# Performance work log

Measured on AMD Instinct MI355X. Metric: run time of the kernel, lower is better.

The kernel has to match this reference:

```python
import jax, jax.numpy as jnp
import numpy as np

B, L, F = 512, 30, 64
N_LEADERS, MAX_LAG = 500, 10
H, TOP_K = 64, 5
SCALE = float(H) ** 0.5


def setup_inputs() -> dict:
    key = jax.random.key(0)
    ks = jax.random.split(key, 16)
    s = 0.05
    return {
        "target_seq": jax.random.normal(ks[0], (B, L, F), jnp.float32),
        "leader_raw_features": jax.random.normal(ks[1], (B, N_LEADERS, MAX_LAG, F), jnp.float32),
        # LSTM params (torch gate order i,f,g,o)
        "W_ih": jax.random.normal(ks[2], (4 * H, F), jnp.float32) * s,
        "W_hh": jax.random.normal(ks[3], (4 * H, H), jnp.float32) * s,
        "b_ih": jax.random.normal(ks[4], (4 * H,), jnp.float32) * s,
        "b_hh": jax.random.normal(ks[5], (4 * H,), jnp.float32) * s,
        # attention projections (bias-free)
        "W_Q": jax.random.normal(ks[6], (H, H), jnp.float32) * s,
        "W_K": jax.random.normal(ks[7], (H, F), jnp.float32) * s,
        # predictor MLP: F->H, H->H//2, H//2->1
        "Wp1": jax.random.normal(ks[8], (H, F), jnp.float32) * s,
        "bp1": jax.random.normal(ks[9], (H,), jnp.float32) * s,
        "Wp2": jax.random.normal(ks[10], (H // 2, H), jnp.float32) * s,
        "bp2": jax.random.normal(ks[11], (H // 2,), jnp.float32) * s,
        "Wp3": jax.random.normal(ks[12], (1, H // 2), jnp.float32) * s,
        "bp3": jax.random.normal(ks[13], (1,), jnp.float32) * s,
    }


def _lstm_last_hidden(x, W_ih, W_hh, b_ih, b_hh):
    # x: [B, L, F] -> last hidden state [B, H]
    b = x.shape[0]
    h0 = jnp.zeros((b, W_hh.shape[1]), x.dtype)

    def step(carry, xt):
        h, c = carry
        gates = xt @ W_ih.T + h @ W_hh.T + b_ih + b_hh  # [B, 4H]
        i, f, g, o = jnp.split(gates, 4, axis=-1)
        i = jax.nn.sigmoid(i)
        f = jax.nn.sigmoid(f)
        g = jnp.tanh(g)
        o = jax.nn.sigmoid(o)
        c = f * c + i * g
        h = o * jnp.tanh(c)
        return (h, c), None

    (h_last, _), _ = jax.lax.scan(step, (h0, h0), jnp.swapaxes(x, 0, 1))
    return h_last


def reference(target_seq, leader_raw_features, W_ih, W_hh, b_ih, b_hh,
              W_Q, W_K, Wp1, bp1, Wp2, bp2, Wp3, bp3):
    b = target_seq.shape[0]
    n_leaders, max_lag, feat = leader_raw_features.shape[1:]

    h_last = _lstm_last_hidden(target_seq, W_ih, W_hh, b_ih, b_hh)  # [B,H]
    query = h_last @ W_Q.T  # [B,H]

    # attn[b,n,l] = sum_h query[b,h] * (W_K @ raw[b,n,l])_h, fused to avoid
    # materializing the [B,N,LAG,H] key tensor.
    attn = jnp.einsum('bnlf,hf,bh->bnl', leader_raw_features, W_K, query) / SCALE

    flat_attn = attn.reshape(b, n_leaders * max_lag)
    k = min(TOP_K, flat_attn.shape[1])
    top_values, top_idx = jax.lax.top_k(flat_attn, k)  # [B,k]
    leader_idx = top_idx // max_lag
    lag_idx = top_idx % max_lag
    top_k_indices = jnp.stack([leader_idx, lag_idx], axis=-1)  # [B,k,2]
    top_k_scores = jax.nn.softmax(top_values, axis=-1)  # [B,k]

    raw_flat = leader_raw_features.reshape(b, n_leaders * max_lag, feat)
    selected = jnp.take_along_axis(raw_flat, top_idx[:, :, None], axis=1)  # [B,k,F]
    weighted = jnp.einsum('bkf,bk->bf', selected, top_k_scores)  # [B,F]

    # predictor MLP (dropout is identity in eval)
    h1 = jax.nn.relu(weighted @ Wp1.T + bp1)
    h2 = jax.nn.relu(h1 @ Wp2.T + bp2)
    pred = h2 @ Wp3.T + bp3  # [B,1]
    return pred, top_k_indices, top_k_scores, attn
```

## Files before the change

### kernel.cpp

```cpp
#include <hip/hip_runtime.h>
#include <math.h>

#define B_SZ   512
#define L_SEQ  30
#define F_DIM  64
#define N_LEAD 500
#define MAXLAG 10
#define H_DIM  64
#define NROWS  5000
#define TOPK   5

#define OFF_IDX   512
#define OFF_SCORE 5632
#define OFF_ATTN  8192

__device__ __forceinline__ float fast_sigmoid(float x) {
    return 1.f / (1.f + __expf(-x));
}
__device__ __forceinline__ float fast_tanh(float x) {
    float ax = fabsf(x);
    float t  = __expf(-2.f * ax);
    float r  = (1.f - t) / (1.f + t);
    return copysignf(r, x);
}
__device__ __forceinline__ float sfl(float v) {
    return __uint_as_float(__builtin_amdgcn_readfirstlane(__float_as_uint(v)));
}

__device__ __forceinline__ float dot16(const float4* __restrict__ w,
                                       const float4* __restrict__ v) {
    float a0 = 0.f, a1 = 0.f, a2 = 0.f, a3 = 0.f;
#pragma unroll
    for (int k = 0; k < 16; k += 4) {
        a0 += w[k+0].x*v[k+0].x + w[k+0].y*v[k+0].y + w[k+0].z*v[k+0].z + w[k+0].w*v[k+0].w;
        a1 += w[k+1].x*v[k+1].x + w[k+1].y*v[k+1].y + w[k+1].z*v[k+1].z + w[k+1].w*v[k+1].w;
        a2 += w[k+2].x*v[k+2].x + w[k+2].y*v[k+2].y + w[k+2].z*v[k+2].z + w[k+2].w*v[k+2].w;
        a3 += w[k+3].x*v[k+3].x + w[k+3].y*v[k+3].y + w[k+3].z*v[k+3].z + w[k+3].w*v[k+3].w;
    }
    return (a0 + a1) + (a2 + a3);
}

__global__ __launch_bounds__(256) void lstm_kq_kernel(
    const float* __restrict__ x,
    const float* __restrict__ W_ih,
    const float* __restrict__ W_hh,
    const float* __restrict__ b_ih,
    const float* __restrict__ b_hh,
    const float* __restrict__ W_Q,
    const float* __restrict__ W_K,
    float* __restrict__ kq)
{
    __shared__ __align__(16) float xs[L_SEQ * F_DIM];
    __shared__ __align__(16) float hs[H_DIM];
    __shared__ __align__(16) float gates[256];

    const int b = blockIdx.x;
    const int t = threadIdx.x;

    for (int i = t; i < L_SEQ * F_DIM; i += 256)
        xs[i] = x[b * L_SEQ * F_DIM + i];
    if (t < H_DIM) hs[t] = 0.f;

    float4 wih[16], whh[16];
    const float4* wihp = (const float4*)(W_ih + t * 64);
    const float4* whhp = (const float4*)(W_hh + t * 64);
#pragma unroll
    for (int k = 0; k < 16; ++k) { wih[k] = wihp[k]; whh[k] = whhp[k]; }
    const float bsum = b_ih[t] + b_hh[t];

    float c = 0.f;
    __syncthreads();

    float gx = bsum + dot16(wih, (const float4*)xs);

    for (int step = 0; step < L_SEQ; ++step) {
        float g = gx + dot16(whh, (const float4*)hs);
        gates[t] = g;
        __syncthreads();
        if (t < H_DIM) {
            float ig = fast_sigmoid(gates[t]);
            float fg = fast_sigmoid(gates[t + 64]);
            float gg = fast_tanh(gates[t + 128]);
            float og = fast_sigmoid(gates[t + 192]);
            c = fg * c + ig * gg;
            hs[t] = og * fast_tanh(c);
        }
        if (step + 1 < L_SEQ)
            gx = bsum + dot16(wih, (const float4*)(xs + (step + 1) * F_DIM));
        __syncthreads();
    }

    if (t < H_DIM)
        gates[t] = dot16((const float4*)(W_Q + t * 64), (const float4*)hs);
    __syncthreads();
    if (t < F_DIM) {
        float a0 = 0.f, a1 = 0.f;
        for (int h = 0; h < H_DIM; h += 2) {
            a0 += gates[h]     * W_K[h * F_DIM + t];
            a1 += gates[h + 1] * W_K[(h + 1) * F_DIM + t];
        }
        kq[b * F_DIM + t] = a0 + a1;
    }
}

__global__ __launch_bounds__(512, 8) void fused_attn_topk_kernel(
    const float* __restrict__ raw,
    const float* __restrict__ kq,
    const float* __restrict__ Wp1, const float* __restrict__ bp1,
    const float* __restrict__ Wp2, const float* __restrict__ bp2,
    const float* __restrict__ Wp3, const float* __restrict__ bp3,
    float* __restrict__ out)
{
    __shared__ float av[NROWS];
    __shared__ float redv[8];
    __shared__ int   redi[8];
    __shared__ float topv[TOPK];
    __shared__ int   topi[TOPK];
    __shared__ float sc[TOPK];
    __shared__ __align__(16) float wsum[64];
    __shared__ __align__(16) float h1[64];
    __shared__ float h2[32];

    const int b = blockIdx.x, t = threadIdx.x;

    const float* kqp = kq + b * 64;
#define LQ(i) const float q##i##x = sfl(kqp[4*(i)+0]), q##i##y = sfl(kqp[4*(i)+1]), \
                          q##i##z = sfl(kqp[4*(i)+2]), q##i##w = sfl(kqp[4*(i)+3]);
    LQ(0) LQ(1) LQ(2) LQ(3) LQ(4) LQ(5) LQ(6) LQ(7)
    LQ(8) LQ(9) LQ(10) LQ(11) LQ(12) LQ(13) LQ(14) LQ(15)
#undef LQ

    float* attn_g = out + OFF_ATTN + (size_t)b * NROWS;
    const float4* p = (const float4*)raw + ((size_t)b * NROWS + t) * 16;

#define DOT4(acc, v, i) acc += v.x*q##i##x + v.y*q##i##y + v.z*q##i##z + v.w*q##i##w;
#define BODY(r) { \
    float4 v0=p[0],v1=p[1],v2=p[2],v3=p[3],v4=p[4],v5=p[5],v6=p[6],v7=p[7]; \
    float s0=0.f,s1=0.f,s2=0.f,s3=0.f; \
    DOT4(s0,v0,0) DOT4(s1,v1,1) DOT4(s2,v2,2) DOT4(s3,v3,3) \
    DOT4(s0,v4,4) DOT4(s1,v5,5) DOT4(s2,v6,6) DOT4(s3,v7,7) \
    v0=p[8];v1=p[9];v2=p[10];v3=p[11];v4=p[12];v5=p[13];v6=p[14];v7=p[15]; \
    DOT4(s0,v0,8)  DOT4(s1,v1,9)  DOT4(s2,v2,10) DOT4(s3,v3,11) \
    DOT4(s0,v4,12) DOT4(s1,v5,13) DOT4(s2,v6,14) DOT4(s3,v7,15) \
    float s = ((s0+s1)+(s2+s3)) * 0.125f; \
    av[r] = s; attn_g[r] = s; }

    int r = t;
#pragma unroll 1
    for (int pass = 0; pass < 9; ++pass) {
        BODY(r)
        r += 512; p += 512 * 16;
    }
    if (r < NROWS) { BODY(r) }
#undef BODY
#undef DOT4
    __syncthreads();

    for (int pp = 0; pp < TOPK; ++pp) {
        float bv = -INFINITY; int bi = 0x7fffffff;
        for (int i = t; i < NROWS; i += 512) {
            float v = av[i];
            if (v > bv || (v == bv && i < bi)) { bv = v; bi = i; }
        }
#pragma unroll
        for (int m = 32; m >= 1; m >>= 1) {
            float ov = __shfl_xor(bv, m);
            int   oi = __shfl_xor(bi, m);
            if (ov > bv || (ov == bv && oi < bi)) { bv = ov; bi = oi; }
        }
        if ((t & 63) == 0) { redv[t >> 6] = bv; redi[t >> 6] = bi; }
        __syncthreads();
        if (t == 0) {
            for (int w = 1; w < 8; ++w)
                if (redv[w] > bv || (redv[w] == bv && redi[w] < bi)) { bv = redv[w]; bi = redi[w]; }
            topv[pp] = bv; topi[pp] = bi;
            av[bi] = -INFINITY;
        }
        __syncthreads();
    }

    if (t == 0) {
        float mx = topv[0];
        float e[TOPK], s = 0.f;
#pragma unroll
        for (int k = 0; k < TOPK; ++k) { e[k] = __expf(topv[k] - mx); s += e[k]; }
        float inv = 1.f / s;
#pragma unroll
        for (int k = 0; k < TOPK; ++k) {
            sc[k] = e[k] * inv;
            out[OFF_IDX + b * 10 + 2 * k]     = (float)(topi[k] / MAXLAG);
            out[OFF_IDX + b * 10 + 2 * k + 1] = (float)(topi[k] % MAXLAG);
            out[OFF_SCORE + b * TOPK + k]     = sc[k];
        }
    }
    __syncthreads();

    if (t < 64) {
        float acc = 0.f;
#pragma unroll
        for (int k = 0; k < TOPK; ++k)
            acc += sc[k] * raw[((size_t)b * NROWS + topi[k]) * 64 + t];
        wsum[t] = acc;
    }
    __syncthreads();
    if (t < 64) {
        float a = bp1[t];
        const float4* w = (const float4*)(Wp1 + t * 64);
        const float4* v = (const float4*)wsum;
#pragma unroll
        for (int k = 0; k < 16; ++k)
            a += w[k].x*v[k].x + w[k].y*v[k].y + w[k].z*v[k].z + w[k].w*v[k].w;
        h1[t] = fmaxf(a, 0.f);
    }
    __syncthreads();
    if (t < 32) {
        float a = bp2[t];
        const float4* w = (const float4*)(Wp2 + t * 64);
        const float4* v = (const float4*)h1;
#pragma unroll
        for (int k = 0; k < 16; ++k)
            a += w[k].x*v[k].x + w[k].y*v[k].y + w[k].z*v[k].z + w[k].w*v[k].w;
        h2[t] = fmaxf(a, 0.f);
    }
    __syncthreads();
    if (t == 0) {
        float a = bp3[0];
#pragma unroll
        for (int f = 0; f < 32; ++f) a += Wp3[f] * h2[f];
        out[b] = a;
    }
}

extern "C" void kernel_launch(void* const* d_in, const int* in_sizes, int n_in,
                              void* d_out, int out_size, void* d_ws, size_t ws_size,
                              hipStream_t stream) {
    const float* target = (const float*)d_in[0];
    const float* raw    = (const float*)d_in[1];
    const float* W_ih   = (const float*)d_in[2];
    const float* W_hh   = (const float*)d_in[3];
    const float* b_ih   = (const float*)d_in[4];
    const float* b_hh   = (const float*)d_in[5];
    const float* W_Q    = (const float*)d_in[6];
    const float* W_K    = (const float*)d_in[7];
    const float* Wp1    = (const float*)d_in[8];
    const float* bp1    = (const float*)d_in[9];
    const float* Wp2    = (const float*)d_in[10];
    const float* bp2    = (const float*)d_in[11];
    const float* Wp3    = (const float*)d_in[12];
    const float* bp3    = (const float*)d_in[13];

    float* out = (float*)d_out;
    float* kq  = (float*)d_ws;

    hipLaunchKernelGGL(lstm_kq_kernel, dim3(B_SZ), dim3(256), 0, stream,
                       target, W_ih, W_hh, b_ih, b_hh, W_Q, W_K, kq);
    hipLaunchKernelGGL(fused_attn_topk_kernel, dim3(B_SZ), dim3(512), 0, stream,
                       raw, kq, Wp1, bp1, Wp2, bp2, Wp3, bp3, out);
}
```

Baseline: 207.2 us.

## Split fused attention/top-k kernel into streaming attn kernel and top-k MLP kernel

The fused per-batch kernel is split in two. The first computes attention scores over the leader features with 4 blocks per batch row, giving 2048 blocks of 256 threads, and writes them to the output buffer. The second reloads those scores into shared memory and runs top-k, softmax and the MLP. The goal is more parallelism and occupancy for the bandwidth-bound streaming pass, which no longer carries a 20KB shared-memory footprint. The cost is an extra kernel launch and a write and re-read of the 10MB attention array.

```diff
diff --git a/kernel.cpp b/kernel.cpp
--- a/kernel.cpp
+++ b/kernel.cpp
@@ -103,17 +103,63 @@
     }
 }
 
-__global__ __launch_bounds__(512, 8) void fused_attn_topk_kernel(
+#define RPB 1250
+__global__ __launch_bounds__(256, 8) void attn_stream_kernel(
+    const float4* __restrict__ raw,
+    const float* __restrict__ kq,
+    float* __restrict__ attn)
+{
+    const int b = blockIdx.x >> 2;
+    const int q = blockIdx.x & 3;
+    const int t = threadIdx.x;
+
+    const float* kqp = kq + b * 64;
+#define LQ(i) const float q##i##x = sfl(kqp[4*(i)+0]), q##i##y = sfl(kqp[4*(i)+1]), \
+                          q##i##z = sfl(kqp[4*(i)+2]), q##i##w = sfl(kqp[4*(i)+3]);
+    LQ(0) LQ(1) LQ(2) LQ(3) LQ(4) LQ(5) LQ(6) LQ(7)
+    LQ(8) LQ(9) LQ(10) LQ(11) LQ(12) LQ(13) LQ(14) LQ(15)
+#undef LQ
+
+    const int row0 = q * RPB;
+    const float4* p = raw + ((size_t)b * NROWS + row0 + t) * 16;
+    float*       ag = attn + (size_t)b * NROWS + row0 + t;
+
+#define DOT4(acc, v, i) acc += v.x*q##i##x + v.y*q##i##y + v.z*q##i##z + v.w*q##i##w;
+#define BODY() { \
+    float4 v0=p[0],v1=p[1],v2=p[2],v3=p[3]; \
+    float s0=0.f,s1=0.f,s2=0.f,s3=0.f; \
+    DOT4(s0,v0,0) DOT4(s1,v1,1) DOT4(s2,v2,2) DOT4(s3,v3,3) \
+    v0=p[4];v1=p[5];v2=p[6];v3=p[7]; \
+    DOT4(s0,v0,4) DOT4(s1,v1,5) DOT4(s2,v2,6) DOT4(s3,v3,7) \
+    v0=p[8];v1=p[9];v2=p[10];v3=p[11]; \
+    DOT4(s0,v0,8) DOT4(s1,v1,9) DOT4(s2,v2,10) DOT4(s3,v3,11) \
+    v0=p[12];v1=p[13];v2=p[14];v3=p[15]; \
+    DOT4(s0,v0,12) DOT4(s1,v1,13) DOT4(s2,v2,14) DOT4(s3,v3,15) \
+    *ag = ((s0+s1)+(s2+s3)) * 0.125f; }
+
+#pragma unroll 1
+    for (int i = 0; i < 4; ++i) {
+        BODY()
+        p += 256 * 16; ag += 256;
+    }
+    if (t < RPB - 1024) {
+        BODY()
+    }
+#undef BODY
+#undef DOT4
+}
+
+__global__ __launch_bounds__(256) void topk_mlp_kernel(
+    const float* __restrict__ attn,
     const float* __restrict__ raw,
-    const float* __restrict__ kq,
     const float* __restrict__ Wp1, const float* __restrict__ bp1,
     const float* __restrict__ Wp2, const float* __restrict__ bp2,
     const float* __restrict__ Wp3, const float* __restrict__ bp3,
     float* __restrict__ out)
 {
-    __shared__ float av[NROWS];
-    __shared__ float redv[8];
-    __shared__ int   redi[8];
+    __shared__ __align__(16) float av[NROWS];
+    __shared__ float redv[4];
+    __shared__ int   redi[4];
     __shared__ float topv[TOPK];
     __shared__ int   topi[TOPK];
     __shared__ float sc[TOPK];
@@ -123,42 +169,14 @@
 
     const int b = blockIdx.x, t = threadIdx.x;
 
-    const float* kqp = kq + b * 64;
-#define LQ(i) const float q##i##x = sfl(kqp[4*(i)+0]), q##i##y = sfl(kqp[4*(i)+1]), \
-                          q##i##z = sfl(kqp[4*(i)+2]), q##i##w = sfl(kqp[4*(i)+3]);
-    LQ(0) LQ(1) LQ(2) LQ(3) LQ(4) LQ(5) LQ(6) LQ(7)
-    LQ(8) LQ(9) LQ(10) LQ(11) LQ(12) LQ(13) LQ(14) LQ(15)
-#undef LQ
-
-    float* attn_g = out + OFF_ATTN + (size_t)b * NROWS;
-    const float4* p = (const float4*)raw + ((size_t)b * NROWS + t) * 16;
-
-#define DOT4(acc, v, i) acc += v.x*q##i##x + v.y*q##i##y + v.z*q##i##z + v.w*q##i##w;
-#define BODY(r) { \
-    float4 v0=p[0],v1=p[1],v2=p[2],v3=p[3],v4=p[4],v5=p[5],v6=p[6],v7=p[7]; \
-    float s0=0.f,s1=0.f,s2=0.f,s3=0.f; \
-    DOT4(s0,v0,0) DOT4(s1,v1,1) DOT4(s2,v2,2) DOT4(s3,v3,3) \
-    DOT4(s0,v4,4) DOT4(s1,v5,5) DOT4(s2,v6,6) DOT4(s3,v7,7) \
-    v0=p[8];v1=p[9];v2=p[10];v3=p[11];v4=p[12];v5=p[13];v6=p[14];v7=p[15]; \
-    DOT4(s0,v0,8)  DOT4(s1,v1,9)  DOT4(s2,v2,10) DOT4(s3,v3,11) \
-    DOT4(s0,v4,12) DOT4(s1,v5,13) DOT4(s2,v6,14) DOT4(s3,v7,15) \
-    float s = ((s0+s1)+(s2+s3)) * 0.125f; \
-    av[r] = s; attn_g[r] = s; }
-
-    int r = t;
-#pragma unroll 1
-    for (int pass = 0; pass < 9; ++pass) {
-        BODY(r)
-        r += 512; p += 512 * 16;
-    }
-    if (r < NROWS) { BODY(r) }
-#undef BODY
-#undef DOT4
+    const float4* ain = (const float4*)(attn + (size_t)b * NROWS);
+    float4* av4 = (float4*)av;
+    for (int i = t; i < NROWS / 4; i += 256) av4[i] = ain[i];
     __syncthreads();
 
     for (int pp = 0; pp < TOPK; ++pp) {
         float bv = -INFINITY; int bi = 0x7fffffff;
-        for (int i = t; i < NROWS; i += 512) {
+        for (int i = t; i < NROWS; i += 256) {
             float v = av[i];
             if (v > bv || (v == bv && i < bi)) { bv = v; bi = i; }
         }
@@ -171,7 +189,7 @@
         if ((t & 63) == 0) { redv[t >> 6] = bv; redi[t >> 6] = bi; }
         __syncthreads();
         if (t == 0) {
-            for (int w = 1; w < 8; ++w)
+            for (int w = 1; w < 4; ++w)
                 if (redv[w] > bv || (redv[w] == bv && redi[w] < bi)) { bv = redv[w]; bi = redi[w]; }
             topv[pp] = bv; topi[pp] = bi;
             av[bi] = -INFINITY;
@@ -249,11 +267,14 @@
     const float* Wp3    = (const float*)d_in[12];
     const float* bp3    = (const float*)d_in[13];
 
-    float* out = (float*)d_out;
-    float* kq  = (float*)d_ws;
+    float* out      = (float*)d_out;
+    float* kq       = (float*)d_ws;
+    float* attn_out = out + OFF_ATTN;
 
     hipLaunchKernelGGL(lstm_kq_kernel, dim3(B_SZ), dim3(256), 0, stream,
                        target, W_ih, W_hh, b_ih, b_hh, W_Q, W_K, kq);
-    hipLaunchKernelGGL(fused_attn_topk_kernel, dim3(B_SZ), dim3(512), 0, stream,
-                       raw, kq, Wp1, bp1, Wp2, bp2, Wp3, bp3, out);
-}
+    hipLaunchKernelGGL(attn_stream_kernel, dim3(B_SZ * 4), dim3(256), 0, stream,
+                       (const float4*)raw, kq, attn_out);
+    hipLaunchKernelGGL(topk_mlp_kernel, dim3(B_SZ), dim3(256), 0, stream,
+                       attn_out, raw, Wp1, bp1, Wp2, bp2, Wp3, bp3, out);
+}
```

Result: slower. 242.6 us (+17.1%).
